# Performance work log

Measured on AMD Instinct MI355X. Metric: run time of the kernel, lower is better.

## Reference

```python
import jax, jax.numpy as jnp
import numpy as np

N_NODES = 50000
N_EDGES = 500000
D_IN = 128
D_HID = 128
OUTPUT_DIM = 10.0


def gcn_conv(x, src, dst, edge_weight, W, b, n_nodes):
    # PyG GCNConv: out = D^{-1/2} (A + I) D^{-1/2} X W + b, self-loop weight 1
    xw = x @ W  # [N, D_out]
    # degree at target nodes, including self-loop weight 1
    deg = jax.ops.segment_sum(edge_weight, dst, num_segments=n_nodes) + 1.0
    dinv = jnp.where(deg > 0, jax.lax.rsqrt(deg), 0.0)  # [N]
    norm = dinv[src] * edge_weight * dinv[dst]  # [E]
    msgs = xw[src] * norm[:, None]  # [E, D_out] gathered+scaled messages
    agg = jax.ops.segment_sum(msgs, dst, num_segments=n_nodes)
    # analytic self-loop contribution: norm_ii = dinv_i * 1 * dinv_i
    agg = agg + xw * (dinv * dinv)[:, None]
    return agg + b


def setup_inputs() -> dict:
    key = jax.random.key(0)
    k = jax.random.split(key, 8)
    x = jax.random.normal(k[0], (N_NODES, D_IN), dtype=jnp.float32)
    edge_index = jax.random.randint(k[1], (2, N_EDGES), 0, N_NODES, dtype=jnp.int64)
    edge_weight = jax.random.uniform(k[2], (N_EDGES,), dtype=jnp.float32)
    s1 = 1.0 / np.sqrt(D_IN)
    s2 = 1.0 / np.sqrt(D_HID)
    W1 = jax.random.uniform(k[3], (D_IN, D_HID), minval=-s1, maxval=s1, dtype=jnp.float32)
    b1 = jnp.zeros((D_HID,), dtype=jnp.float32)
    W2 = jax.random.uniform(k[4], (D_HID, D_HID), minval=-s2, maxval=s2, dtype=jnp.float32)
    b2 = jnp.zeros((D_HID,), dtype=jnp.float32)
    Wf = jax.random.uniform(k[5], (D_HID, 1), minval=-s2, maxval=s2, dtype=jnp.float32)
    bf = jax.random.uniform(k[6], (1,), minval=-s2, maxval=s2, dtype=jnp.float32)
    return {"x": x, "edge_index": edge_index, "edge_weight": edge_weight,
            "W1": W1, "b1": b1, "W2": W2, "b2": b2, "Wf": Wf, "bf": bf}


def reference(x, edge_index, edge_weight, W1, b1, W2, b2, Wf, bf):
    src, dst = edge_index[0], edge_index[1]
    h = gcn_conv(x, src, dst, edge_weight, W1, b1, N_NODES)
    h = gcn_conv(h, src, dst, edge_weight, W2, b2, N_NODES)
    out = h @ Wf + bf  # [N, 1]
    return jax.nn.sigmoid(out) * OUTPUT_DIM
```

## Files before the change

### kernel.cpp

```cpp
#include <hip/hip_runtime.h>

#define N_NODES 50000
#define N_EDGES 500000
#define D 128
#define FXS 4194304.0f
#define CAP 64

typedef unsigned long long u64;

__global__ void pass1_kernel(const int* __restrict__ src, const int* __restrict__ dst,
                             const float* __restrict__ ew,
                             const float* __restrict__ W1, const float* __restrict__ W2,
                             const float* __restrict__ b1, const float* __restrict__ b2,
                             const float* __restrict__ Wf, const float* __restrict__ bf,
                             u64* __restrict__ degcnt, int2* __restrict__ pairs,
                             float* __restrict__ v, float* __restrict__ consts,
                             int eb) {
    if ((int)blockIdx.x == eb) {
        __shared__ float u[D];
        int t = threadIdx.x;
        if (t < D) {
            float a = 0.f;
#pragma unroll 8
            for (int j = 0; j < D; ++j) a += W2[t * D + j] * Wf[j];
            u[t] = a;
        }
        __syncthreads();
        if (t < D) {
            float a = 0.f;
#pragma unroll 8
            for (int k = 0; k < D; ++k) a += W1[t * D + k] * u[k];
            v[t] = a;
        }
        if (t == 0) {
            float c = 0.f;
            for (int k = 0; k < D; ++k) c += b1[k] * u[k];
            consts[0] = c;
        } else if (t == 1) {
            float c = bf[0];
            for (int k = 0; k < D; ++k) c += b2[k] * Wf[k];
            consts[1] = c;
        }
        return;
    }
    int e = blockIdx.x * blockDim.x + threadIdx.x;
    if (e < N_EDGES) {
        int d = dst[e];
        float w = ew[e];
        unsigned fx = __float2uint_rn(w * FXS);
        u64 old = atomicAdd(&degcnt[d], (1ull << 32) | (u64)fx);
        int slot = (int)(old >> 32);
        if (slot < CAP)
            pairs[d * CAP + slot] = make_int2(src[e], __float_as_int(w));
    }
}

__global__ void gemv_kernel(const float* __restrict__ x, const float* __restrict__ v,
                            const u64* __restrict__ degcnt,
                            float* __restrict__ dinv, float* __restrict__ tw,
                            int* __restrict__ cntv) {
    __shared__ float vs[D];
    const int t = threadIdx.x;
    if (t < D) vs[t] = v[t];
    __syncthreads();
    const int lane = t & 63;
    const int n = blockIdx.x * 4 + (t >> 6);
    float2 xv = ((const float2*)(x + (size_t)n * D))[lane];
    float a = xv.x * vs[lane * 2] + xv.y * vs[lane * 2 + 1];
#pragma unroll
    for (int off = 32; off > 0; off >>= 1) a += __shfl_xor(a, off);
    if (lane == 0) {
        u64 dc = degcnt[n];
        int c = (int)(dc >> 32);
        float deg = (float)(unsigned)(dc & 0xffffffffu) * (1.0f / FXS);
        float di = rsqrtf(deg + 1.0f);
        dinv[n] = di;
        cntv[n] = (c < CAP) ? c : CAP;
        tw[n] = di * a;
    }
}

__global__ void gather_s_kernel(const float* __restrict__ tw, const float* __restrict__ dinv,
                                const int* __restrict__ cntv, const int2* __restrict__ pairs,
                                const float* __restrict__ consts, float* __restrict__ sw) {
    int tid = threadIdx.x;
    int n = blockIdx.x * 32 + (tid >> 3);
    int l = tid & 7;
    if (n >= N_NODES) return;
    int cnt = cntv[n];
    const int2* row = pairs + (size_t)n * CAP;
    float acc = 0.f;
    for (int i = l; i < cnt; i += 8) {
        int2 p = row[i];
        acc += __int_as_float(p.y) * tw[p.x];
    }
    acc += __shfl_xor(acc, 1);
    acc += __shfl_xor(acc, 2);
    acc += __shfl_xor(acc, 4);
    if (l == 0) {
        float di = dinv[n];
        float s = di * (acc + tw[n]) + consts[0];
        sw[n] = di * s;
    }
}

__global__ void gather_z_kernel(const float* __restrict__ sw, const float* __restrict__ dinv,
                                const int* __restrict__ cntv, const int2* __restrict__ pairs,
                                const float* __restrict__ consts, float* __restrict__ out) {
    int tid = threadIdx.x;
    int n = blockIdx.x * 32 + (tid >> 3);
    int l = tid & 7;
    if (n >= N_NODES) return;
    int cnt = cntv[n];
    const int2* row = pairs + (size_t)n * CAP;
    float acc = 0.f;
    for (int i = l; i < cnt; i += 8) {
        int2 p = row[i];
        acc += __int_as_float(p.y) * sw[p.x];
    }
    acc += __shfl_xor(acc, 1);
    acc += __shfl_xor(acc, 2);
    acc += __shfl_xor(acc, 4);
    if (l == 0) {
        float di = dinv[n];
        float z = di * (acc + sw[n]) + consts[1];
        out[n] = 10.0f / (1.0f + expf(-z));
    }
}

extern "C" void kernel_launch(void* const* d_in, const int* in_sizes, int n_in,
                              void* d_out, int out_size, void* d_ws, size_t ws_size,
                              hipStream_t stream) {
    const float* x  = (const float*)d_in[0];
    const int*   ei = (const int*)d_in[1];
    const float* ew = (const float*)d_in[2];
    const float* W1 = (const float*)d_in[3];
    const float* b1 = (const float*)d_in[4];
    const float* W2 = (const float*)d_in[5];
    const float* b2 = (const float*)d_in[6];
    const float* Wf = (const float*)d_in[7];
    const float* bf = (const float*)d_in[8];
    const int* srcv = ei;
    const int* dstv = ei + N_EDGES;
    float* out = (float*)d_out;

    char* p = (char*)d_ws;
    auto alloc = [&](size_t bytes) { void* r = (void*)p; p += (bytes + 255) & ~(size_t)255; return r; };
    u64*   degcnt = (u64*)alloc((size_t)N_NODES * 8);
    float* dinv   = (float*)alloc(N_NODES * 4);
    int*   cntv   = (int*)alloc(N_NODES * 4);
    float* tw     = (float*)alloc(N_NODES * 4);
    float* sw     = (float*)alloc(N_NODES * 4);
    float* v      = (float*)alloc(D * 4);
    float* consts = (float*)alloc(2 * 4);
    int2*  pairs  = (int2*)alloc((size_t)N_NODES * CAP * 8);

    const int EB = (N_EDGES + 255) / 256;

    hipMemsetAsync(degcnt, 0, (size_t)N_NODES * 8, stream);

    pass1_kernel<<<EB + 1, 256, 0, stream>>>(srcv, dstv, ew, W1, W2, b1, b2, Wf, bf,
                                             degcnt, pairs, v, consts, EB);

    gemv_kernel<<<N_NODES / 4, 256, 0, stream>>>(x, v, degcnt, dinv, tw, cntv);

    gather_s_kernel<<<(N_NODES + 31) / 32, 256, 0, stream>>>(tw, dinv, cntv, pairs, consts, sw);
    gather_z_kernel<<<(N_NODES + 31) / 32, 256, 0, stream>>>(sw, dinv, cntv, pairs, consts, out);
}
```

Baseline: 137.4 us.

## Replace bucketed CSR gather with per-edge float atomic scatter passes

Drops the fixed-capacity per-destination pair buckets, which were filled with 64-bit packed atomics, in favour of plain float atomic degree accumulation. Each of the two propagation layers now runs an edge-parallel scatter kernel doing atomicAdd into node accumulators, followed by a small per-node finalize kernel. This removes the 25.6MB pair buffer and the CAP truncation, but adds atomic contention, two extra launches, and order-dependent float summation.

Result: slower. 186.5 us (+35.7%).

```diff
diff --git a/kernel.cpp b/kernel.cpp
--- a/kernel.cpp
+++ b/kernel.cpp
@@ -3,19 +3,13 @@
 #define N_NODES 50000
 #define N_EDGES 500000
 #define D 128
-#define FXS 4194304.0f
-#define CAP 64
 
-typedef unsigned long long u64;
-
-__global__ void pass1_kernel(const int* __restrict__ src, const int* __restrict__ dst,
-                             const float* __restrict__ ew,
+__global__ void pass1_kernel(const int* __restrict__ dst, const float* __restrict__ ew,
                              const float* __restrict__ W1, const float* __restrict__ W2,
                              const float* __restrict__ b1, const float* __restrict__ b2,
                              const float* __restrict__ Wf, const float* __restrict__ bf,
-                             u64* __restrict__ degcnt, int2* __restrict__ pairs,
-                             float* __restrict__ v, float* __restrict__ consts,
-                             int eb) {
+                             float* __restrict__ deg,
+                             float* __restrict__ v, float* __restrict__ consts, int eb) {
     if ((int)blockIdx.x == eb) {
         __shared__ float u[D];
         int t = threadIdx.x;
@@ -44,21 +38,13 @@
         return;
     }
     int e = blockIdx.x * blockDim.x + threadIdx.x;
-    if (e < N_EDGES) {
-        int d = dst[e];
-        float w = ew[e];
-        unsigned fx = __float2uint_rn(w * FXS);
-        u64 old = atomicAdd(&degcnt[d], (1ull << 32) | (u64)fx);
-        int slot = (int)(old >> 32);
-        if (slot < CAP)
-            pairs[d * CAP + slot] = make_int2(src[e], __float_as_int(w));
-    }
+    if (e < N_EDGES) unsafeAtomicAdd(&deg[dst[e]], ew[e]);
 }
 
 __global__ void gemv_kernel(const float* __restrict__ x, const float* __restrict__ v,
-                            const u64* __restrict__ degcnt,
+                            const float* __restrict__ deg,
                             float* __restrict__ dinv, float* __restrict__ tw,
-                            int* __restrict__ cntv) {
+                            float* __restrict__ sacc) {
     __shared__ float vs[D];
     const int t = threadIdx.x;
     if (t < D) vs[t] = v[t];
@@ -70,60 +56,38 @@
 #pragma unroll
     for (int off = 32; off > 0; off >>= 1) a += __shfl_xor(a, off);
     if (lane == 0) {
-        u64 dc = degcnt[n];
-        int c = (int)(dc >> 32);
-        float deg = (float)(unsigned)(dc & 0xffffffffu) * (1.0f / FXS);
-        float di = rsqrtf(deg + 1.0f);
+        float di = rsqrtf(deg[n] + 1.0f);
+        float twv = di * a;
         dinv[n] = di;
-        cntv[n] = (c < CAP) ? c : CAP;
-        tw[n] = di * a;
+        tw[n] = twv;
+        sacc[n] = twv;
     }
 }
 
-__global__ void gather_s_kernel(const float* __restrict__ tw, const float* __restrict__ dinv,
-                                const int* __restrict__ cntv, const int2* __restrict__ pairs,
-                                const float* __restrict__ consts, float* __restrict__ sw) {
-    int tid = threadIdx.x;
-    int n = blockIdx.x * 32 + (tid >> 3);
-    int l = tid & 7;
-    if (n >= N_NODES) return;
-    int cnt = cntv[n];
-    const int2* row = pairs + (size_t)n * CAP;
-    float acc = 0.f;
-    for (int i = l; i < cnt; i += 8) {
-        int2 p = row[i];
-        acc += __int_as_float(p.y) * tw[p.x];
-    }
-    acc += __shfl_xor(acc, 1);
-    acc += __shfl_xor(acc, 2);
-    acc += __shfl_xor(acc, 4);
-    if (l == 0) {
+__global__ void scatter_kernel(const int* __restrict__ src, const int* __restrict__ dst,
+                               const float* __restrict__ ew, const float* __restrict__ val,
+                               float* __restrict__ acc) {
+    int e = blockIdx.x * blockDim.x + threadIdx.x;
+    if (e < N_EDGES) unsafeAtomicAdd(&acc[dst[e]], ew[e] * val[src[e]]);
+}
+
+__global__ void fin_s_kernel(const float* __restrict__ sacc, const float* __restrict__ dinv,
+                             const float* __restrict__ consts, float* __restrict__ sw,
+                             float* __restrict__ zacc) {
+    int n = blockIdx.x * blockDim.x + threadIdx.x;
+    if (n < N_NODES) {
         float di = dinv[n];
-        float s = di * (acc + tw[n]) + consts[0];
-        sw[n] = di * s;
+        float v = di * (di * sacc[n] + consts[0]);
+        sw[n] = v;
+        zacc[n] = v;
     }
 }
 
-__global__ void gather_z_kernel(const float* __restrict__ sw, const float* __restrict__ dinv,
-                                const int* __restrict__ cntv, const int2* __restrict__ pairs,
-                                const float* __restrict__ consts, float* __restrict__ out) {
-    int tid = threadIdx.x;
-    int n = blockIdx.x * 32 + (tid >> 3);
-    int l = tid & 7;
-    if (n >= N_NODES) return;
-    int cnt = cntv[n];
-    const int2* row = pairs + (size_t)n * CAP;
-    float acc = 0.f;
-    for (int i = l; i < cnt; i += 8) {
-        int2 p = row[i];
-        acc += __int_as_float(p.y) * sw[p.x];
-    }
-    acc += __shfl_xor(acc, 1);
-    acc += __shfl_xor(acc, 2);
-    acc += __shfl_xor(acc, 4);
-    if (l == 0) {
-        float di = dinv[n];
-        float z = di * (acc + sw[n]) + consts[1];
+__global__ void fin_z_kernel(const float* __restrict__ zacc, const float* __restrict__ dinv,
+                             const float* __restrict__ consts, float* __restrict__ out) {
+    int n = blockIdx.x * blockDim.x + threadIdx.x;
+    if (n < N_NODES) {
+        float z = dinv[n] * zacc[n] + consts[1];
         out[n] = 10.0f / (1.0f + expf(-z));
     }
 }
@@ -146,24 +110,28 @@
 
     char* p = (char*)d_ws;
     auto alloc = [&](size_t bytes) { void* r = (void*)p; p += (bytes + 255) & ~(size_t)255; return r; };
-    u64*   degcnt = (u64*)alloc((size_t)N_NODES * 8);
+    float* deg    = (float*)alloc(N_NODES * 4);
     float* dinv   = (float*)alloc(N_NODES * 4);
-    int*   cntv   = (int*)alloc(N_NODES * 4);
     float* tw     = (float*)alloc(N_NODES * 4);
+    float* sacc   = (float*)alloc(N_NODES * 4);
     float* sw     = (float*)alloc(N_NODES * 4);
+    float* zacc   = (float*)alloc(N_NODES * 4);
     float* v      = (float*)alloc(D * 4);
     float* consts = (float*)alloc(2 * 4);
-    int2*  pairs  = (int2*)alloc((size_t)N_NODES * CAP * 8);
 
     const int EB = (N_EDGES + 255) / 256;
+    const int NB = (N_NODES + 255) / 256;
 
-    hipMemsetAsync(degcnt, 0, (size_t)N_NODES * 8, stream);
+    hipMemsetAsync(deg, 0, N_NODES * 4, stream);
 
-    pass1_kernel<<<EB + 1, 256, 0, stream>>>(srcv, dstv, ew, W1, W2, b1, b2, Wf, bf,
-                                             degcnt, pairs, v, consts, EB);
+    pass1_kernel<<<EB + 1, 256, 0, stream>>>(dstv, ew, W1, W2, b1, b2, Wf, bf,
+                                             deg, v, consts, EB);
 
-    gemv_kernel<<<N_NODES / 4, 256, 0, stream>>>(x, v, degcnt, dinv, tw, cntv);
+    gemv_kernel<<<N_NODES / 4, 256, 0, stream>>>(x, v, deg, dinv, tw, sacc);
 
-    gather_s_kernel<<<(N_NODES + 31) / 32, 256, 0, stream>>>(tw, dinv, cntv, pairs, consts, sw);
-    gather_z_kernel<<<(N_NODES + 31) / 32, 256, 0, stream>>>(sw, dinv, cntv, pairs, consts, out);
+    scatter_kernel<<<EB, 256, 0, stream>>>(srcv, dstv, ew, tw, sacc);
+    fin_s_kernel<<<NB, 256, 0, stream>>>(sacc, dinv, consts, sw, zacc);
+
+    scatter_kernel<<<EB, 256, 0, stream>>>(srcv, dstv, ew, sw, zacc);
+    fin_z_kernel<<<NB, 256, 0, stream>>>(zacc, dinv, consts, out);
 }
```

## Fuse edge scatter with x·v GEMV, pack edge pairs into 32 bits

Applied to the files above, without the earlier changes.

The edge-bucketing pass and the node GEMV now run as one kernel split by block index, so the two independent memory streams can overlap. The memset is replaced by an init kernel that also computes the collapsed weight vector, and a small epilogue kernel derives dinv and tw. Edge pairs are packed into 32 bits (16-bit src index, 16-bit quantized weight), halving the scatter and gather traffic. That packing loses weight precision, and a 16-bit src field cannot hold node ids up to 50000 once shifted into a 32-bit word, so src indices above 65535 would be truncated (ids below 65536 do fit).

New measurement: 139.2 us. About the same (+1.3%).

```diff
diff --git a/kernel.cpp b/kernel.cpp
--- a/kernel.cpp
+++ b/kernel.cpp
@@ -7,16 +7,14 @@
 #define CAP 64
 
 typedef unsigned long long u64;
+typedef unsigned int uint;
 
-__global__ void pass1_kernel(const int* __restrict__ src, const int* __restrict__ dst,
-                             const float* __restrict__ ew,
-                             const float* __restrict__ W1, const float* __restrict__ W2,
-                             const float* __restrict__ b1, const float* __restrict__ b2,
-                             const float* __restrict__ Wf, const float* __restrict__ bf,
-                             u64* __restrict__ degcnt, int2* __restrict__ pairs,
-                             float* __restrict__ v, float* __restrict__ consts,
-                             int eb) {
-    if ((int)blockIdx.x == eb) {
+__global__ void init_kernel(const float* __restrict__ W1, const float* __restrict__ W2,
+                            const float* __restrict__ b1, const float* __restrict__ b2,
+                            const float* __restrict__ Wf, const float* __restrict__ bf,
+                            u64* __restrict__ degcnt, float* __restrict__ v,
+                            float* __restrict__ consts, int zb) {
+    if ((int)blockIdx.x == zb) {
         __shared__ float u[D];
         int t = threadIdx.x;
         if (t < D) {
@@ -43,56 +41,71 @@
         }
         return;
     }
-    int e = blockIdx.x * blockDim.x + threadIdx.x;
-    if (e < N_EDGES) {
-        int d = dst[e];
-        float w = ew[e];
-        unsigned fx = __float2uint_rn(w * FXS);
-        u64 old = atomicAdd(&degcnt[d], (1ull << 32) | (u64)fx);
-        int slot = (int)(old >> 32);
-        if (slot < CAP)
-            pairs[d * CAP + slot] = make_int2(src[e], __float_as_int(w));
+    int i = blockIdx.x * 256 + threadIdx.x;
+    if (i < N_NODES) degcnt[i] = 0;
+}
+
+__global__ void fused_kernel(const int* __restrict__ src, const int* __restrict__ dst,
+                             const float* __restrict__ ew, const float* __restrict__ x,
+                             const float* __restrict__ v,
+                             u64* __restrict__ degcnt, uint* __restrict__ pairs,
+                             float* __restrict__ tvec, int eb) {
+    int b = blockIdx.x;
+    if (b < eb) {
+        int e = b * 256 + threadIdx.x;
+        if (e < N_EDGES) {
+            int d = dst[e];
+            float w = ew[e];
+            unsigned fx = __float2uint_rn(w * FXS);
+            u64 old = atomicAdd(&degcnt[d], (1ull << 32) | (u64)fx);
+            int slot = (int)(old >> 32);
+            uint pk = ((uint)src[e] << 16) | (uint)__float2uint_rn(w * 65535.0f);
+            if (slot < CAP)
+                pairs[d * CAP + slot] = pk;
+        }
+    } else {
+        __shared__ float vs[D];
+        const int t = threadIdx.x;
+        if (t < D) vs[t] = v[t];
+        __syncthreads();
+        const int lane = t & 63;
+        const int n = (b - eb) * 4 + (t >> 6);
+        float2 xv = ((const float2*)(x + (size_t)n * D))[lane];
+        float a = xv.x * vs[lane * 2] + xv.y * vs[lane * 2 + 1];
+#pragma unroll
+        for (int off = 32; off > 0; off >>= 1) a += __shfl_xor(a, off);
+        if (lane == 0) tvec[n] = a;
     }
 }
 
-__global__ void gemv_kernel(const float* __restrict__ x, const float* __restrict__ v,
-                            const u64* __restrict__ degcnt,
-                            float* __restrict__ dinv, float* __restrict__ tw,
-                            int* __restrict__ cntv) {
-    __shared__ float vs[D];
-    const int t = threadIdx.x;
-    if (t < D) vs[t] = v[t];
-    __syncthreads();
-    const int lane = t & 63;
-    const int n = blockIdx.x * 4 + (t >> 6);
-    float2 xv = ((const float2*)(x + (size_t)n * D))[lane];
-    float a = xv.x * vs[lane * 2] + xv.y * vs[lane * 2 + 1];
-#pragma unroll
-    for (int off = 32; off > 0; off >>= 1) a += __shfl_xor(a, off);
-    if (lane == 0) {
+__global__ void epi_kernel(const u64* __restrict__ degcnt, const float* __restrict__ tvec,
+                           float* __restrict__ dinv, float* __restrict__ tw,
+                           int* __restrict__ cntv) {
+    int n = blockIdx.x * blockDim.x + threadIdx.x;
+    if (n < N_NODES) {
         u64 dc = degcnt[n];
         int c = (int)(dc >> 32);
         float deg = (float)(unsigned)(dc & 0xffffffffu) * (1.0f / FXS);
         float di = rsqrtf(deg + 1.0f);
         dinv[n] = di;
         cntv[n] = (c < CAP) ? c : CAP;
-        tw[n] = di * a;
+        tw[n] = di * tvec[n];
     }
 }
 
 __global__ void gather_s_kernel(const float* __restrict__ tw, const float* __restrict__ dinv,
-                                const int* __restrict__ cntv, const int2* __restrict__ pairs,
+                                const int* __restrict__ cntv, const uint* __restrict__ pairs,
                                 const float* __restrict__ consts, float* __restrict__ sw) {
     int tid = threadIdx.x;
     int n = blockIdx.x * 32 + (tid >> 3);
     int l = tid & 7;
     if (n >= N_NODES) return;
     int cnt = cntv[n];
-    const int2* row = pairs + (size_t)n * CAP;
+    const uint* row = pairs + (size_t)n * CAP;
     float acc = 0.f;
     for (int i = l; i < cnt; i += 8) {
-        int2 p = row[i];
-        acc += __int_as_float(p.y) * tw[p.x];
+        uint p = row[i];
+        acc += (float)(p & 0xffffu) * (1.0f / 65535.0f) * tw[p >> 16];
     }
     acc += __shfl_xor(acc, 1);
     acc += __shfl_xor(acc, 2);
@@ -105,18 +118,18 @@
 }
 
 __global__ void gather_z_kernel(const float* __restrict__ sw, const float* __restrict__ dinv,
-                                const int* __restrict__ cntv, const int2* __restrict__ pairs,
+                                const int* __restrict__ cntv, const uint* __restrict__ pairs,
                                 const float* __restrict__ consts, float* __restrict__ out) {
     int tid = threadIdx.x;
     int n = blockIdx.x * 32 + (tid >> 3);
     int l = tid & 7;
     if (n >= N_NODES) return;
     int cnt = cntv[n];
-    const int2* row = pairs + (size_t)n * CAP;
+    const uint* row = pairs + (size_t)n * CAP;
     float acc = 0.f;
     for (int i = l; i < cnt; i += 8) {
-        int2 p = row[i];
-        acc += __int_as_float(p.y) * sw[p.x];
+        uint p = row[i];
+        acc += (float)(p & 0xffffu) * (1.0f / 65535.0f) * sw[p >> 16];
     }
     acc += __shfl_xor(acc, 1);
     acc += __shfl_xor(acc, 2);
@@ -149,20 +162,22 @@
     u64*   degcnt = (u64*)alloc((size_t)N_NODES * 8);
     float* dinv   = (float*)alloc(N_NODES * 4);
     int*   cntv   = (int*)alloc(N_NODES * 4);
+    float* tvec   = (float*)alloc(N_NODES * 4);
     float* tw     = (float*)alloc(N_NODES * 4);
     float* sw     = (float*)alloc(N_NODES * 4);
     float* v      = (float*)alloc(D * 4);
     float* consts = (float*)alloc(2 * 4);
-    int2*  pairs  = (int2*)alloc((size_t)N_NODES * CAP * 8);
+    uint*  pairs  = (uint*)alloc((size_t)N_NODES * CAP * 4);
 
     const int EB = (N_EDGES + 255) / 256;
+    const int NB = (N_NODES + 255) / 256;
 
-    hipMemsetAsync(degcnt, 0, (size_t)N_NODES * 8, stream);
+    init_kernel<<<NB + 1, 256, 0, stream>>>(W1, W2, b1, b2, Wf, bf, degcnt, v, consts, NB);
 
-    pass1_kernel<<<EB + 1, 256, 0, stream>>>(srcv, dstv, ew, W1, W2, b1, b2, Wf, bf,
-                                             degcnt, pairs, v, consts, EB);
+    fused_kernel<<<EB + N_NODES / 4, 256, 0, stream>>>(srcv, dstv, ew, x, v,
+                                                       degcnt, pairs, tvec, EB);
 
-    gemv_kernel<<<N_NODES / 4, 256, 0, stream>>>(x, v, degcnt, dinv, tw, cntv);
+    epi_kernel<<<NB, 256, 0, stream>>>(degcnt, tvec, dinv, tw, cntv);
 
     gather_s_kernel<<<(N_NODES + 31) / 32, 256, 0, stream>>>(tw, dinv, cntv, pairs, consts, sw);
     gather_z_kernel<<<(N_NODES + 31) / 32, 256, 0, stream>>>(sw, dinv, cntv, pairs, consts, out);
```
